# Optimization experiments

Measured on AMD Instinct MI355X. Metric: run time of the kernel, lower is better.

## Reference

```python
import jax, jax.numpy as jnp
import numpy as np

B, S, D, H = 2, 2048, 1024, 16
HD = D // H  # head_dim = 64


def setup_inputs() -> dict:
    key = jax.random.key(0)
    ks = jax.random.split(key, 7)
    s = 0.02
    return {
        "queries": jax.random.normal(ks[0], (B, S, D), jnp.float32),
        "keys": jax.random.normal(ks[1], (B, S, D), jnp.float32),
        "values": jax.random.normal(ks[2], (B, S, D), jnp.float32),
        "Wq": jax.random.normal(ks[3], (D, D), jnp.float32) * s,
        "Wk": jax.random.normal(ks[4], (D, D), jnp.float32) * s,
        "Wv": jax.random.normal(ks[5], (D, D), jnp.float32) * s,
        "Wo": jax.random.normal(ks[6], (D, D), jnp.float32) * s,
    }


def reference(queries, keys, values, Wq, Wk, Wv, Wo):
    # Projections (torch Linear: x @ W.T); split into heads -> [B, H, S, HD]
    def split_heads(x):
        b, s, _ = x.shape
        return x.reshape(b, s, H, HD).transpose(0, 2, 1, 3)

    q = split_heads(queries @ Wq.T)
    k = split_heads(keys @ Wk.T)
    v = split_heads(values @ Wv.T)

    scale = 1.0 / jnp.sqrt(jnp.asarray(HD, q.dtype))
    scores = jnp.einsum("bhqd,bhkd->bhqk", q, k) * scale  # [B,H,S,S]
    attn = jax.nn.softmax(scores, axis=-1)
    ctx = jnp.einsum("bhqk,bhkd->bhqd", attn, v)  # [B,H,S,HD]
    out = ctx.transpose(0, 2, 1, 3).reshape(queries.shape[0], -1, D)
    return out @ Wo.T
```

## Files before the change

### kernel.cpp

```cpp
#include <hip/hip_runtime.h>
#include <hip/hip_bf16.h>


#define B_ 2
#define S_ 2048
#define D_ 1024
#define H_ 16
#define HD_ 64
#define NE_ (B_ * S_ * D_)
#define WN_ (D_ * D_)

typedef unsigned short u16;
typedef unsigned int u32;
typedef u16 __attribute__((may_alias)) u16_ma;
typedef float __attribute__((may_alias)) f32_ma;
typedef u32 v4u __attribute__((ext_vector_type(4)));
typedef v4u __attribute__((may_alias)) v4u_ma;
typedef short bf16x8 __attribute__((ext_vector_type(8)));
typedef bf16x8 __attribute__((may_alias)) bf16x8_ma;
typedef float f32x4 __attribute__((ext_vector_type(4)));
typedef float f32x16 __attribute__((ext_vector_type(16)));

__device__ __forceinline__ float bf2f(u16 u) {
  u32 x = ((u32)u) << 16;
  return __builtin_bit_cast(float, x);
}
__device__ __forceinline__ u16 f2bf(float f) {
  __hip_bfloat16 h = __float2bfloat16(f);
  return __builtin_bit_cast(u16, h);
}
__device__ __forceinline__ u32 pk2(u32 alo, u32 ahi) {
  return (u32)f2bf(__builtin_bit_cast(float, alo)) |
         ((u32)f2bf(__builtin_bit_cast(float, ahi)) << 16);
}
__device__ __forceinline__ u32 pkf(float lo, float hi) {
  return (u32)f2bf(lo) | ((u32)f2bf(hi) << 16);
}

__device__ __forceinline__ void gl_lds16(const u16* g, u16* l) {
  auto gp = (const __attribute__((address_space(1))) unsigned int*)(const void*)g;
  auto lp = (__attribute__((address_space(3))) unsigned int*)(void*)l;
  __builtin_amdgcn_global_load_lds(gp, lp, 16, 0, 0);
}

__device__ __forceinline__ bool detect_f32(const u16* Wg) {
  const int lane = threadIdx.x & 63;
  bool hit = false;
#pragma unroll
  for (int i = 0; i < 4; ++i) {
    v4u u = *(const v4u_ma*)(Wg + lane * 32 + i * 8);
#pragma unroll
    for (int j = 0; j < 4; ++j) {
      u32 w = u[j];
      hit |= (((w >> 7) & 0xFFu) >= 0xF0u) || (((w >> 23) & 0xFFu) >= 0xF0u);
    }
  }
  return __any(hit);
}

__global__ __launch_bounds__(256) void convert_bf16(
    const void* s0, const void* s1, const void* s2, const void* s3,
    const void* s4, const void* s5, const void* s6, u16* __restrict__ dst_in,
    u16* __restrict__ dst_w, const u16* __restrict__ Wdet) {
  const bool det = detect_f32(Wdet);
  const int y = blockIdx.y;
  const void* src;
  u16* dst;
  int n;
  if (y < 3) {
    src = (y == 0) ? s0 : ((y == 1) ? s1 : s2);
    dst = dst_in + (size_t)y * NE_;
    n = NE_;
  } else {
    src = (y == 3) ? s3 : ((y == 4) ? s4 : ((y == 5) ? s5 : s6));
    dst = dst_w + (size_t)(y - 3) * WN_;
    n = WN_;
  }
  const int i = (blockIdx.x * 256 + threadIdx.x) * 8;
  if (i >= n) return;
  v4u out;
  if (det) {
    const v4u_ma* fp = (const v4u_ma*)((const float*)src + i);
    v4u f0 = fp[0], f1 = fp[1];
    out[0] = pk2(f0[0], f0[1]);
    out[1] = pk2(f0[2], f0[3]);
    out[2] = pk2(f1[0], f1[1]);
    out[3] = pk2(f1[2], f1[3]);
  } else {
    out = *(const v4u_ma*)((const u16*)src + i);
  }
  *(v4u_ma*)(dst + i) = out;
}

template <int BN, bool OUT_DET>
__global__ __launch_bounds__(256) void proj_g(
    const u16* __restrict__ Ab, const u16* __restrict__ Wb,
    void* __restrict__ Cb, const u16* __restrict__ Wdet) {
  __shared__ u16 Al[128 * 64];
  __shared__ u16 Wl[BN * 64];

  const bool outf32 = OUT_DET ? detect_f32(Wdet) : false;

  const int tid = threadIdx.x;
  const int lane = tid & 63, wid = tid >> 6;
  const int lg = lane >> 4, li = lane & 15;
  const int wr = wid >> 1, wc = wid & 1;
  const int z = blockIdx.z;
  const char* Ag = (const char*)(Ab + (size_t)z * NE_);
  const char* Wg = (const char*)(Wb + (size_t)z * WN_);
  const int m0 = blockIdx.x * 128, n0 = blockIdx.y * BN;

  const int lr = lane >> 3;
  const int swzb = ((lane & 7) * 16) ^ (lr << 4);

  constexpr int NF = BN / 32;
  f32x4 acc[4][NF];
#pragma unroll
  for (int m = 0; m < 4; ++m)
#pragma unroll
    for (int n = 0; n < NF; ++n) acc[m][n] = (f32x4){0.f, 0.f, 0.f, 0.f};

  for (int kt = 0; kt < 16; ++kt) {
    const int k0b = kt * 128;
    __syncthreads();
#pragma unroll
    for (int c = 0; c < 4; ++c) {
      const int row = wid * 32 + c * 8 + lr;
      gl_lds16((const u16*)(Ag + (size_t)(m0 + row) * 2048 + k0b + swzb),
               Al + (wid * 32 + c * 8) * 64);
    }
    if constexpr (BN == 128) {
#pragma unroll
      for (int c = 0; c < 4; ++c) {
        const int row = wid * 32 + c * 8 + lr;
        gl_lds16((const u16*)(Wg + (size_t)(n0 + row) * 2048 + k0b + swzb),
                 Wl + (wid * 32 + c * 8) * 64);
      }
    } else {
#pragma unroll
      for (int c = 0; c < 2; ++c) {
        const int row = wid * 16 + c * 8 + lr;
        gl_lds16((const u16*)(Wg + (size_t)(n0 + row) * 2048 + k0b + swzb),
                 Wl + (wid * 16 + c * 8) * 64);
      }
    }
    __syncthreads();

#pragma unroll
    for (int ks = 0; ks < 2; ++ks) {
      bf16x8 af[4], bw[NF];
#pragma unroll
      for (int m = 0; m < 4; ++m) {
        const int row = wr * 64 + m * 16 + li;
        af[m] = *(const bf16x8_ma*)((const char*)Al + row * 128 +
                                    ((ks * 64 + lg * 16) ^ ((row & 7) << 4)));
      }
#pragma unroll
      for (int n = 0; n < NF; ++n) {
        const int row = wc * (BN / 2) + n * 16 + li;
        bw[n] = *(const bf16x8_ma*)((const char*)Wl + row * 128 +
                                    ((ks * 64 + lg * 16) ^ ((row & 7) << 4)));
      }
#pragma unroll
      for (int m = 0; m < 4; ++m)
#pragma unroll
        for (int n = 0; n < NF; ++n)
          acc[m][n] = __builtin_amdgcn_mfma_f32_16x16x32_bf16(af[m], bw[n],
                                                              acc[m][n], 0, 0, 0);
    }
  }

  const float zs = (!OUT_DET && z == 0) ? 0.125f : 1.0f;
#pragma unroll
  for (int m = 0; m < 4; ++m)
#pragma unroll
    for (int n = 0; n < NF; ++n)
#pragma unroll
      for (int r = 0; r < 4; ++r) {
        const int row = m0 + wr * 64 + m * 16 + lg * 4 + r;
        const int col = n0 + wc * (BN / 2) + n * 16 + li;
        const size_t idx = (size_t)row * D_ + col;
        const float v = acc[m][n][r] * zs;
        if (OUT_DET) {
          if (outf32)
            ((f32_ma*)Cb)[idx] = v;
          else
            ((u16_ma*)Cb)[idx] = f2bf(v);
        } else {
          ((u16_ma*)((u16*)Cb + (size_t)z * NE_))[idx] = f2bf(v);
        }
      }
}

__global__ __launch_bounds__(256) void attn3(
    const u16* __restrict__ Qg, const u16* __restrict__ Kg,
    const u16* __restrict__ Vg, u16* __restrict__ Og) {
  __shared__ u16 Kl[2][64 * 64];
  __shared__ u16 VTl[2][64 * 64];

  const int tid = threadIdx.x;
  const int wid = tid >> 6, lane = tid & 63;
  const int l31 = lane & 31;
  const int hi = lane >> 5;

  const int bid = blockIdx.x;
  const int swz = (bid & 7) * 64 + (bid >> 3);
  const int qb = swz & 15;
  const int h = (swz >> 4) & 15;
  const int b = swz >> 8;
  const size_t bbase = (size_t)b * S_ * D_;
  const int hoff = h * HD_;
  const int q0w = qb * 128 + wid * 32;

  bf16x8 bq[4];
  {
    const u16* qp = Qg + bbase + (size_t)(q0w + l31) * D_ + hoff + hi * 8;
#pragma unroll
    for (int dblk = 0; dblk < 4; ++dblk)
      bq[dblk] = *(const bf16x8_ma*)(qp + dblk * 16);
  }

  f32x16 o0, o1;
#pragma unroll
  for (int i = 0; i < 16; ++i) {
    o0[i] = 0.f;
    o1[i] = 0.f;
  }
  float mrun = -1e30f, lrun = 0.f;

  const int krr = tid >> 3;
  const int kc8 = (tid & 7) * 8;
  const int vkr = lane;
  const int vd0 = wid * 8;

  v4u kr0, kr1, vr0, vr1;
  auto kv_load = [&](int kt) {
    const int key0 = kt * 64;
    kr0 = *(const v4u_ma*)(Kg + bbase + (size_t)(key0 + krr) * D_ + hoff + kc8);
    kr1 = *(const v4u_ma*)(Kg + bbase + (size_t)(key0 + 32 + krr) * D_ + hoff + kc8);
    vr0 = *(const v4u_ma*)(Vg + bbase + (size_t)(key0 + vkr) * D_ + hoff + vd0);
    vr1 = *(const v4u_ma*)(Vg + bbase + (size_t)(key0 + vkr) * D_ + hoff + vd0 + 32);
  };
  auto kv_write = [&](int bi) {
    char* Kb = (char*)&Kl[bi][0];
    char* Vb = (char*)&VTl[bi][0];
    const int ksw = (krr & 7) << 4;
    *(v4u_ma*)(Kb + krr * 128 + ((kc8 * 2) ^ ksw)) = kr0;
    *(v4u_ma*)(Kb + (32 + krr) * 128 + ((kc8 * 2) ^ ksw)) = kr1;
    union {
      v4u v;
      u16 e[8];
    } uu;
    uu.v = vr0;
#pragma unroll
    for (int j = 0; j < 8; ++j) {
      const int d = vd0 + j;
      *(u16*)(Vb + d * 128 + ((vkr * 2) ^ ((d & 7) << 4))) = uu.e[j];
    }
    uu.v = vr1;
#pragma unroll
    for (int j = 0; j < 8; ++j) {
      const int d = vd0 + 32 + j;
      *(u16*)(Vb + d * 128 + ((vkr * 2) ^ ((d & 7) << 4))) = uu.e[j];
    }
  };

  kv_load(0);
  kv_write(0);

  const int swk = (l31 & 7) << 4;

  for (int kt = 0; kt < S_ / 64; ++kt) {
    __syncthreads();
    if (kt < S_ / 64 - 1) kv_load(kt + 1);

    const char* Kb = (const char*)&Kl[kt & 1][0];
    const char* Vb = (const char*)&VTl[kt & 1][0];

    f32x16 sT0, sT1;
#pragma unroll
    for (int i = 0; i < 16; ++i) {
      sT0[i] = 0.f;
      sT1[i] = 0.f;
    }
    __builtin_amdgcn_s_setprio(1);
#pragma unroll
    for (int dblk = 0; dblk < 4; ++dblk) {
      const int cb = (dblk * 32 + hi * 16);
      bf16x8 a0 = *(const bf16x8_ma*)(Kb + l31 * 128 + (cb ^ swk));
      bf16x8 a1 = *(const bf16x8_ma*)(Kb + (32 + l31) * 128 + (cb ^ swk));
      sT0 = __builtin_amdgcn_mfma_f32_32x32x16_bf16(a0, bq[dblk], sT0, 0, 0, 0);
      sT1 = __builtin_amdgcn_mfma_f32_32x32x16_bf16(a1, bq[dblk], sT1, 0, 0, 0);
    }
    __builtin_amdgcn_s_setprio(0);

    float pmax = sT0[0];
#pragma unroll
    for (int i = 0; i < 7; ++i)
      pmax = fmaxf(fmaxf(pmax, sT0[2 * i + 1]), sT0[2 * i + 2]);
    pmax = fmaxf(pmax, sT0[15]);
#pragma unroll
    for (int i = 0; i < 8; ++i)
      pmax = fmaxf(fmaxf(pmax, sT1[2 * i]), sT1[2 * i + 1]);
    pmax = fmaxf(pmax, __shfl_xor(pmax, 32));
    if (!__all(pmax - mrun <= 8.0f)) {
      const float mnew = fmaxf(mrun, pmax);
      const float al = __expf(mrun - mnew);
      mrun = mnew;
      lrun *= al;
      o0 *= al;
      o1 *= al;
    }

    u32 w[16];
    float sum = 0.f;
#pragma unroll
    for (int kh = 0; kh < 2; ++kh)
#pragma unroll
      for (int g = 0; g < 4; ++g)
#pragma unroll
        for (int u = 0; u < 2; ++u) {
          const int r = g * 4 + 2 * u;
          const float pe = __expf((kh ? sT1[r] : sT0[r]) - mrun);
          const float po = __expf((kh ? sT1[r + 1] : sT0[r + 1]) - mrun);
          sum += pe + po;
          w[kh * 8 + g * 2 + u] = pkf(pe, po);
        }
    sum += __shfl_xor(sum, 32);
    lrun += sum;

    bf16x8 pf[4];
#pragma unroll
    for (int km = 0; km < 4; ++km) {
      const int a = 4 * km;
      const u32 s0 = hi ? w[a] : w[a + 2];
      const u32 s1 = hi ? w[a + 1] : w[a + 3];
      const u32 r0 = (u32)__shfl_xor((int)s0, 32);
      const u32 r1 = (u32)__shfl_xor((int)s1, 32);
      union {
        u32 d[4];
        bf16x8 v;
      } uu;
      uu.d[0] = hi ? r0 : w[a];
      uu.d[1] = hi ? r1 : w[a + 1];
      uu.d[2] = hi ? w[a + 2] : r0;
      uu.d[3] = hi ? w[a + 3] : r1;
      pf[km] = uu.v;
    }

    __builtin_amdgcn_s_setprio(1);
#pragma unroll
    for (int km = 0; km < 4; ++km) {
      const int cb = (km * 32 + hi * 16);
      bf16x8 v0 = *(const bf16x8_ma*)(Vb + l31 * 128 + (cb ^ swk));
      bf16x8 v1 = *(const bf16x8_ma*)(Vb + (32 + l31) * 128 + (cb ^ swk));
      o0 = __builtin_amdgcn_mfma_f32_32x32x16_bf16(v0, pf[km], o0, 0, 0, 0);
      o1 = __builtin_amdgcn_mfma_f32_32x32x16_bf16(v1, pf[km], o1, 0, 0, 0);
    }
    __builtin_amdgcn_s_setprio(0);

    if (kt < S_ / 64 - 1) kv_write((kt + 1) & 1);
  }

  const float inv = 1.f / lrun;
  u16* orow = Og + bbase + (size_t)(q0w + l31) * D_ + hoff;
#pragma unroll
  for (int r = 0; r < 16; ++r) {
    const int d0 = (r & 3) + 8 * (r >> 2) + 4 * hi;
    orow[d0] = f2bf(o0[r] * inv);
    orow[d0 + 32] = f2bf(o1[r] * inv);
  }
}

template <bool A_SCR, bool SCR_F32, bool OUT_FINAL>
__global__ __launch_bounds__(256) void proj_slow(
    const void* __restrict__ Ag, const u16* __restrict__ Wg,
    void* __restrict__ Cg) {
  const bool det = detect_f32(Wg);
  const bool a_f32 = A_SCR ? SCR_F32 : det;
  const int m = blockIdx.x;
  const int n = blockIdx.y * 256 + threadIdx.x;
  const size_t arow = (size_t)m * D_;
  const size_t wrow = (size_t)n * D_;
  float acc = 0.f;
  for (int k = 0; k < D_; ++k) {
    float a = a_f32 ? ((const f32_ma*)Ag)[arow + k]
                    : bf2f(((const u16_ma*)Ag)[arow + k]);
    float w = det ? ((const f32_ma*)Wg)[wrow + k]
                  : bf2f(((const u16_ma*)Wg)[wrow + k]);
    acc += a * w;
  }
  const size_t ci = (size_t)m * D_ + n;
  const bool c_f32 = OUT_FINAL ? det : SCR_F32;
  if (c_f32)
    ((f32_ma*)Cg)[ci] = acc;
  else
    ((u16_ma*)Cg)[ci] = f2bf(acc);
}

template <bool SCR_F32>
__global__ __launch_bounds__(256) void attn_slow(
    const void* __restrict__ Qg, const void* __restrict__ Kg,
    const void* __restrict__ Vg, void* __restrict__ Cg) {
  const int tid = threadIdx.x;
  const int qblk = blockIdx.x & 7;
  const int h = (blockIdx.x >> 3) & 15;
  const int b = blockIdx.x >> 7;
  const int q = qblk * 256 + tid;
  const size_t base = (size_t)b * S_ * D_;
  const int hoff = h * HD_;
  float qv[64];
  {
    const size_t qrow = base + (size_t)q * D_ + hoff;
    for (int d = 0; d < 64; ++d)
      qv[d] = SCR_F32 ? ((const f32_ma*)Qg)[qrow + d]
                      : bf2f(((const u16_ma*)Qg)[qrow + d]);
  }
  float o[64];
  for (int d = 0; d < 64; ++d) o[d] = 0.f;
  float m = -1e30f, l = 0.f;
  for (int key = 0; key < S_; ++key) {
    const size_t krow = base + (size_t)key * D_ + hoff;
    float s = 0.f;
    for (int d = 0; d < 64; ++d) {
      float kx = SCR_F32 ? ((const f32_ma*)Kg)[krow + d]
                         : bf2f(((const u16_ma*)Kg)[krow + d]);
      s += qv[d] * kx;
    }
    s *= 0.125f;
    float mn = fmaxf(m, s);
    float al = expf(m - mn);
    float pe = expf(s - mn);
    m = mn;
    l = l * al + pe;
    for (int d = 0; d < 64; ++d) {
      float vx = SCR_F32 ? ((const f32_ma*)Vg)[krow + d]
                         : bf2f(((const u16_ma*)Vg)[krow + d]);
      o[d] = o[d] * al + pe * vx;
    }
  }
  const float il = 1.f / l;
  const size_t crow = base + (size_t)q * D_ + hoff;
  for (int d = 0; d < 64; ++d) {
    if (SCR_F32)
      ((f32_ma*)Cg)[crow + d] = o[d] * il;
    else
      ((u16_ma*)Cg)[crow + d] = f2bf(o[d] * il);
  }
}

extern "C" void kernel_launch(void* const* d_in, const int* in_sizes, int n_in,
                              void* d_out, int out_size, void* d_ws,
                              size_t ws_size, hipStream_t stream) {
  const u16* Wdet = (const u16*)d_in[3];
  dim3 blk(256);

  if (ws_size >= (size_t)4 * NE_ * sizeof(float)) {
    u16* Qi = (u16*)d_ws;
    u16* Wc = Qi + (size_t)3 * NE_;
    u16* Qp = Wc + (size_t)4 * WN_;
    u16* Xp = Qp + (size_t)3 * NE_;

    convert_bf16<<<dim3(2048, 7), blk, 0, stream>>>(
        d_in[0], d_in[1], d_in[2], d_in[3], d_in[4], d_in[5], d_in[6], Qi, Wc,
        Wdet);
    proj_g<128, false><<<dim3(32, 8, 3), blk, 0, stream>>>(Qi, Wc, Qp, Wdet);
    attn3<<<dim3(512), blk, 0, stream>>>(Qp, Qp + NE_, Qp + (size_t)2 * NE_, Xp);
    proj_g<64, true><<<dim3(32, 16, 1), blk, 0, stream>>>(
        Xp, Wc + (size_t)3 * WN_, d_out, Wdet);
  } else {
    dim3 gproj(B_ * S_, D_ / 256);
    dim3 gattn(B_ * H_ * (S_ / 256));
    u16* Qp = (u16*)d_out;
    u16* Kp = (u16*)d_in[0];
    u16* Vp = (u16*)d_in[1];
    u16* Xp = (u16*)d_in[2];
    proj_slow<false, false, false><<<gproj, blk, 0, stream>>>(
        d_in[0], (const u16*)d_in[3], Qp);
    proj_slow<false, false, false><<<gproj, blk, 0, stream>>>(
        d_in[1], (const u16*)d_in[4], Kp);
    proj_slow<false, false, false><<<gproj, blk, 0, stream>>>(
        d_in[2], (const u16*)d_in[5], Vp);
    attn_slow<false><<<gattn, blk, 0, stream>>>(Qp, Kp, Vp, Xp);
    proj_slow<true, false, true><<<gproj, blk, 0, stream>>>(
        Xp, (const u16*)d_in[6], d_out);
  }
}
```

Measured before the change: 232.3 us.

## Double-buffer projection GEMM loads and use manual RNE bf16 packing

Projection GEMM now double-buffers its LDS tiles, issuing the next K-tile's global-to-LDS loads before computing the current one, and uses vmcnt waits with raw barriers. The bf16 conversions are replaced with a bit-trick round-to-nearest-even to cut conversion instructions in the epilogues and softmax packing. The convert kernel returns early when inputs are already bf16, reading them directly in the projection. Doubling LDS may lower occupancy, and the manual rounding does not handle NaN specially.

```diff
diff --git a/kernel.cpp b/kernel.cpp
--- a/kernel.cpp
+++ b/kernel.cpp
@@ -29,12 +29,21 @@
   __hip_bfloat16 h = __float2bfloat16(f);
   return __builtin_bit_cast(u16, h);
 }
+__device__ __forceinline__ u16 rne1(float f) {
+  u32 a = __builtin_bit_cast(u32, f);
+  a += 0x7FFFu + ((a >> 16) & 1u);
+  return (u16)(a >> 16);
+}
+__device__ __forceinline__ u32 rne_pair(float lo, float hi) {
+  u32 a = __builtin_bit_cast(u32, lo);
+  u32 b = __builtin_bit_cast(u32, hi);
+  a += 0x7FFFu + ((a >> 16) & 1u);
+  b += 0x7FFFu + ((b >> 16) & 1u);
+  return (a >> 16) | (b & 0xFFFF0000u);
+}
 __device__ __forceinline__ u32 pk2(u32 alo, u32 ahi) {
   return (u32)f2bf(__builtin_bit_cast(float, alo)) |
          ((u32)f2bf(__builtin_bit_cast(float, ahi)) << 16);
-}
-__device__ __forceinline__ u32 pkf(float lo, float hi) {
-  return (u32)f2bf(lo) | ((u32)f2bf(hi) << 16);
 }
 
 __device__ __forceinline__ void gl_lds16(const u16* g, u16* l) {
@@ -63,6 +72,7 @@
     const void* s4, const void* s5, const void* s6, u16* __restrict__ dst_in,
     u16* __restrict__ dst_w, const u16* __restrict__ Wdet) {
   const bool det = detect_f32(Wdet);
+  if (!det) return;
   const int y = blockIdx.y;
   const void* src;
   u16* dst;
@@ -78,73 +88,99 @@
   }
   const int i = (blockIdx.x * 256 + threadIdx.x) * 8;
   if (i >= n) return;
+  const v4u_ma* fp = (const v4u_ma*)((const float*)src + i);
+  v4u f0 = fp[0], f1 = fp[1];
   v4u out;
-  if (det) {
-    const v4u_ma* fp = (const v4u_ma*)((const float*)src + i);
-    v4u f0 = fp[0], f1 = fp[1];
-    out[0] = pk2(f0[0], f0[1]);
-    out[1] = pk2(f0[2], f0[3]);
-    out[2] = pk2(f1[0], f1[1]);
-    out[3] = pk2(f1[2], f1[3]);
-  } else {
-    out = *(const v4u_ma*)((const u16*)src + i);
-  }
+  out[0] = pk2(f0[0], f0[1]);
+  out[1] = pk2(f0[2], f0[3]);
+  out[2] = pk2(f1[0], f1[1]);
+  out[3] = pk2(f1[2], f1[3]);
   *(v4u_ma*)(dst + i) = out;
 }
 
 template <int BN, bool OUT_DET>
 __global__ __launch_bounds__(256) void proj_g(
-    const u16* __restrict__ Ab, const u16* __restrict__ Wb,
-    void* __restrict__ Cb, const u16* __restrict__ Wdet) {
-  __shared__ u16 Al[128 * 64];
-  __shared__ u16 Wl[BN * 64];
-
-  const bool outf32 = OUT_DET ? detect_f32(Wdet) : false;
+    const u16* __restrict__ Asc, const u16* __restrict__ Wsc,
+    void* __restrict__ Cb, const u16* __restrict__ Wdet,
+    const u16* __restrict__ Ao0, const u16* __restrict__ Ao1,
+    const u16* __restrict__ Ao2, const u16* __restrict__ Wo0,
+    const u16* __restrict__ Wo1, const u16* __restrict__ Wo2) {
+  __shared__ u16 Al[2][128 * 64];
+  __shared__ u16 Wl[2][BN * 64];
+
+  const bool det = detect_f32(Wdet);
+  const int z = blockIdx.z;
+
+  const u16* Aptr;
+  const u16* Wptr;
+  if (OUT_DET) {
+    Aptr = Asc;
+    Wptr = det ? Wsc : Wo0;
+  } else {
+    Aptr = det ? (Asc + (size_t)z * NE_)
+               : (z == 0 ? Ao0 : (z == 1 ? Ao1 : Ao2));
+    Wptr = det ? (Wsc + (size_t)z * WN_)
+               : (z == 0 ? Wo0 : (z == 1 ? Wo1 : Wo2));
+  }
+  const char* Ag = (const char*)Aptr;
+  const char* Wg = (const char*)Wptr;
 
   const int tid = threadIdx.x;
   const int lane = tid & 63, wid = tid >> 6;
   const int lg = lane >> 4, li = lane & 15;
   const int wr = wid >> 1, wc = wid & 1;
-  const int z = blockIdx.z;
-  const char* Ag = (const char*)(Ab + (size_t)z * NE_);
-  const char* Wg = (const char*)(Wb + (size_t)z * WN_);
   const int m0 = blockIdx.x * 128, n0 = blockIdx.y * BN;
 
   const int lr = lane >> 3;
   const int swzb = ((lane & 7) * 16) ^ (lr << 4);
 
-  constexpr int NF = BN / 32;
-  f32x4 acc[4][NF];
-#pragma unroll
-  for (int m = 0; m < 4; ++m)
-#pragma unroll
-    for (int n = 0; n < NF; ++n) acc[m][n] = (f32x4){0.f, 0.f, 0.f, 0.f};
-
-  for (int kt = 0; kt < 16; ++kt) {
+  auto issue = [&](int bi, int kt) {
     const int k0b = kt * 128;
-    __syncthreads();
 #pragma unroll
     for (int c = 0; c < 4; ++c) {
       const int row = wid * 32 + c * 8 + lr;
       gl_lds16((const u16*)(Ag + (size_t)(m0 + row) * 2048 + k0b + swzb),
-               Al + (wid * 32 + c * 8) * 64);
+               &Al[bi][(wid * 32 + c * 8) * 64]);
     }
     if constexpr (BN == 128) {
 #pragma unroll
       for (int c = 0; c < 4; ++c) {
         const int row = wid * 32 + c * 8 + lr;
         gl_lds16((const u16*)(Wg + (size_t)(n0 + row) * 2048 + k0b + swzb),
-                 Wl + (wid * 32 + c * 8) * 64);
+                 &Wl[bi][(wid * 32 + c * 8) * 64]);
       }
     } else {
 #pragma unroll
       for (int c = 0; c < 2; ++c) {
         const int row = wid * 16 + c * 8 + lr;
         gl_lds16((const u16*)(Wg + (size_t)(n0 + row) * 2048 + k0b + swzb),
-                 Wl + (wid * 16 + c * 8) * 64);
+                 &Wl[bi][(wid * 16 + c * 8) * 64]);
       }
     }
-    __syncthreads();
+  };
+
+  constexpr int NF = BN / 32;
+  f32x4 acc[4][NF];
+#pragma unroll
+  for (int m = 0; m < 4; ++m)
+#pragma unroll
+    for (int n = 0; n < NF; ++n) acc[m][n] = (f32x4){0.f, 0.f, 0.f, 0.f};
+
+  issue(0, 0);
+
+  for (int kt = 0; kt < 16; ++kt) {
+    const int cur = kt & 1;
+    if (kt < 15) {
+      issue(cur ^ 1, kt + 1);
+      if constexpr (BN == 128)
+        asm volatile("s_waitcnt vmcnt(8)" ::: "memory");
+      else
+        asm volatile("s_waitcnt vmcnt(6)" ::: "memory");
+    } else {
+      asm volatile("s_waitcnt vmcnt(0)" ::: "memory");
+    }
+    __builtin_amdgcn_s_barrier();
+    asm volatile("" ::: "memory");
 
 #pragma unroll
     for (int ks = 0; ks < 2; ++ks) {
@@ -152,13 +188,13 @@
 #pragma unroll
       for (int m = 0; m < 4; ++m) {
         const int row = wr * 64 + m * 16 + li;
-        af[m] = *(const bf16x8_ma*)((const char*)Al + row * 128 +
+        af[m] = *(const bf16x8_ma*)((const char*)&Al[cur][0] + row * 128 +
                                     ((ks * 64 + lg * 16) ^ ((row & 7) << 4)));
       }
 #pragma unroll
       for (int n = 0; n < NF; ++n) {
         const int row = wc * (BN / 2) + n * 16 + li;
-        bw[n] = *(const bf16x8_ma*)((const char*)Wl + row * 128 +
+        bw[n] = *(const bf16x8_ma*)((const char*)&Wl[cur][0] + row * 128 +
                                     ((ks * 64 + lg * 16) ^ ((row & 7) << 4)));
       }
 #pragma unroll
@@ -168,8 +204,12 @@
           acc[m][n] = __builtin_amdgcn_mfma_f32_16x16x32_bf16(af[m], bw[n],
                                                               acc[m][n], 0, 0, 0);
     }
-  }
-
+
+    asm volatile("" ::: "memory");
+    __builtin_amdgcn_s_barrier();
+  }
+
+  const bool outf32 = OUT_DET ? det : false;
   const float zs = (!OUT_DET && z == 0) ? 0.125f : 1.0f;
 #pragma unroll
   for (int m = 0; m < 4; ++m)
@@ -185,9 +225,9 @@
           if (outf32)
             ((f32_ma*)Cb)[idx] = v;
           else
-            ((u16_ma*)Cb)[idx] = f2bf(v);
+            ((u16_ma*)Cb)[idx] = rne1(v);
         } else {
-          ((u16_ma*)((u16*)Cb + (size_t)z * NE_))[idx] = f2bf(v);
+          ((u16_ma*)((u16*)Cb + (size_t)z * NE_))[idx] = rne1(v);
         }
       }
 }
@@ -324,7 +364,7 @@
           const float pe = __expf((kh ? sT1[r] : sT0[r]) - mrun);
           const float po = __expf((kh ? sT1[r + 1] : sT0[r + 1]) - mrun);
           sum += pe + po;
-          w[kh * 8 + g * 2 + u] = pkf(pe, po);
+          w[kh * 8 + g * 2 + u] = rne_pair(pe, po);
         }
     sum += __shfl_xor(sum, 32);
     lrun += sum;
@@ -367,8 +407,8 @@
 #pragma unroll
   for (int r = 0; r < 16; ++r) {
     const int d0 = (r & 3) + 8 * (r >> 2) + 4 * hi;
-    orow[d0] = f2bf(o0[r] * inv);
-    orow[d0 + 32] = f2bf(o1[r] * inv);
+    orow[d0] = rne1(o0[r] * inv);
+    orow[d0 + 32] = rne1(o1[r] * inv);
   }
 }
 
@@ -464,10 +504,14 @@
     convert_bf16<<<dim3(2048, 7), blk, 0, stream>>>(
         d_in[0], d_in[1], d_in[2], d_in[3], d_in[4], d_in[5], d_in[6], Qi, Wc,
         Wdet);
-    proj_g<128, false><<<dim3(32, 8, 3), blk, 0, stream>>>(Qi, Wc, Qp, Wdet);
+    proj_g<128, false><<<dim3(32, 8, 3), blk, 0, stream>>>(
+        Qi, Wc, Qp, Wdet, (const u16*)d_in[0], (const u16*)d_in[1],
+        (const u16*)d_in[2], (const u16*)d_in[3], (const u16*)d_in[4],
+        (const u16*)d_in[5]);
     attn3<<<dim3(512), blk, 0, stream>>>(Qp, Qp + NE_, Qp + (size_t)2 * NE_, Xp);
     proj_g<64, true><<<dim3(32, 16, 1), blk, 0, stream>>>(
-        Xp, Wc + (size_t)3 * WN_, d_out, Wdet);
+        Xp, Wc + (size_t)3 * WN_, d_out, Wdet, nullptr, nullptr, nullptr,
+        (const u16*)d_in[6], nullptr, nullptr);
   } else {
     dim3 gproj(B_ * S_, D_ / 256);
     dim3 gattn(B_ * H_ * (S_ / 256));
```

New measurement: 231.1 us. About the same (-0.5%).
